# Kernel tuning notes

Hardware: AMD Instinct MI355X
Metric: run time of the kernel (lower is better)

## Reference

```python
import jax, jax.numpy as jnp
import numpy as np

BS = 128
E4M3_MAX = 448.0
E5M2_MAX = 57344.0


def qdq(x, fmax, dt):
    # block-wise (128-wide, last dim) fp8 quantize + dequantize (simulates act_quant + dequant in fp8_gemm)
    *lead, K = x.shape
    xb = x.reshape(*lead, K // BS, BS)
    s = jnp.maximum(jnp.max(jnp.abs(xb), axis=-1, keepdims=True) / fmax, 1e-12)
    xq = (xb / s).astype(dt).astype(jnp.float32)
    return (xq * s).reshape(*lead, K)


def fp8_linear(x, w, w_scale, fmax, dt, bias=None):
    # weight is fp8-valued (stored as f32 of the rounded values) with per-output-row-block scales
    x_dq = qdq(x, fmax, dt)
    sv = jnp.repeat(w_scale, BS)[: w.shape[0]]
    y = jnp.einsum('btk,ok->bto', x_dq, w * sv[:, None])
    return y if bias is None else y + bias


def fp8_ln(x, g, gs, b, bsc, eps=1e-5):
    mean = jnp.mean(x, axis=-1, keepdims=True)
    var = jnp.mean(jnp.square(x - mean), axis=-1, keepdims=True)  # unbiased=False
    xn = (x - mean) / jnp.sqrt(var + eps)
    d = x.shape[-1]
    return xn * (g * jnp.repeat(gs, BS)[:d]) + (b * jnp.repeat(bsc, BS)[:d])


def _fwd(x, attn_mask, wq, qs, wk, ks, wv, vs, wo, os_, fc1_w, fc1_s, fc1_b, fc2_w, fc2_s, fc2_b,
         ln1_g, ln1_gs, ln1_b, ln1_bs, ln2_g, ln2_gs, ln2_b, ln2_bs):
    B, T, C = x.shape
    H = 16
    HD = C // H
    e5 = jnp.float8_e5m2
    # attention (q/k/v/out projections use E5M2 fp8)
    q = fp8_linear(x, wq, qs, E5M2_MAX, e5).reshape(B, T, H, HD).transpose(0, 2, 1, 3)
    k = fp8_linear(x, wk, ks, E5M2_MAX, e5).reshape(B, T, H, HD).transpose(0, 2, 1, 3)
    v = fp8_linear(x, wv, vs, E5M2_MAX, e5).reshape(B, T, H, HD).transpose(0, 2, 1, 3)
    scores = jnp.einsum('bhqd,bhkd->bhqk', q, k) / jnp.sqrt(jnp.float32(HD))
    scores = jnp.where(attn_mask[:, None] == 0, -jnp.inf, scores)
    attn = jax.nn.softmax(scores, axis=-1)  # dropout = identity (eval)
    ctx = jnp.einsum('bhqk,bhkd->bhqd', attn, v).transpose(0, 2, 1, 3).reshape(B, T, C)
    attn_out = fp8_linear(ctx, wo, os_, E5M2_MAX, e5)
    x = fp8_ln(x + attn_out, ln1_g, ln1_gs, ln1_b, ln1_bs)
    # MLP (E4M3 fp8)
    e4 = jnp.float8_e4m3fn
    h = fp8_linear(x, fc1_w, fc1_s, E4M3_MAX, e4, fc1_b)
    h = jax.nn.gelu(h, approximate=False)  # torch nn.GELU default = exact erf
    ffn = fp8_linear(h, fc2_w, fc2_s, E4M3_MAX, e4, fc2_b)
    x = fp8_ln(x + ffn, ln2_g, ln2_gs, ln2_b, ln2_bs)
    return x


def _xavier_fp8(key, out_f, in_f, dt):
    bound = float(np.sqrt(6.0 / (in_f + out_f)))
    w = jax.random.uniform(key, (out_f, in_f), jnp.float32, -bound, bound)
    return w.astype(dt).astype(jnp.float32)  # simulate fp8 storage


def setup_inputs() -> dict:
    key = jax.random.key(0)
    kk = jax.random.split(key, 8)
    B, T, C, MLP = 2, 1024, 2048, 8192
    e5, e4 = jnp.float8_e5m2, jnp.float8_e4m3fn
    x = jax.random.normal(kk[0], (B, T, C), jnp.float32)
    attn_mask = jnp.broadcast_to(jnp.tril(jnp.ones((T, T), jnp.int32))[None], (B, T, T))
    nb = C // BS  # 16
    inp = {
        'x': x,
        'attn_mask': attn_mask,
        'wq': _xavier_fp8(kk[1], C, C, e5), 'qs': jnp.ones(nb, jnp.float32),
        'wk': _xavier_fp8(kk[2], C, C, e5), 'ks': jnp.ones(nb, jnp.float32),
        'wv': _xavier_fp8(kk[3], C, C, e5), 'vs': jnp.ones(nb, jnp.float32),
        'wo': _xavier_fp8(kk[4], C, C, e5), 'os_': jnp.ones(nb, jnp.float32),
        'fc1_w': _xavier_fp8(kk[5], MLP, C, e4), 'fc1_s': jnp.ones(MLP // BS, jnp.float32), 'fc1_b': jnp.zeros(MLP, jnp.float32),
        'fc2_w': _xavier_fp8(kk[6], C, MLP, e4), 'fc2_s': jnp.ones(nb, jnp.float32), 'fc2_b': jnp.zeros(C, jnp.float32),
        'ln1_g': jnp.ones(C, jnp.float32), 'ln1_gs': jnp.ones(nb, jnp.float32),
        'ln1_b': jnp.zeros(C, jnp.float32), 'ln1_bs': jnp.ones(nb, jnp.float32),
        'ln2_g': jnp.ones(C, jnp.float32), 'ln2_gs': jnp.ones(nb, jnp.float32),
        'ln2_b': jnp.zeros(C, jnp.float32), 'ln2_bs': jnp.ones(nb, jnp.float32),
    }
    return inp


def reference(x, attn_mask, wq, qs, wk, ks, wv, vs, wo, os_, fc1_w, fc1_s, fc1_b, fc2_w, fc2_s, fc2_b,
              ln1_g, ln1_gs, ln1_b, ln1_bs, ln2_g, ln2_gs, ln2_b, ln2_bs):
    return _fwd(x, attn_mask, wq, qs, wk, ks, wv, vs, wo, os_, fc1_w, fc1_s, fc1_b, fc2_w, fc2_s, fc2_b,
                ln1_g, ln1_gs, ln1_b, ln1_bs, ln2_g, ln2_gs, ln2_b, ln2_bs)
```

## Files before the change

### kernel.cpp

```cpp
#include <hip/hip_runtime.h>
#include <cstdint>


typedef __bf16 bf16x8 __attribute__((ext_vector_type(8)));
typedef unsigned short u16x8 __attribute__((ext_vector_type(8)));
typedef float f32x4 __attribute__((ext_vector_type(4)));
typedef float f32x16 __attribute__((ext_vector_type(16)));
typedef int i32x8 __attribute__((ext_vector_type(8)));
typedef unsigned short u16;

#if __has_builtin(__builtin_amdgcn_exp2f)
#define EXP2F(x) __builtin_amdgcn_exp2f(x)
#else
#define EXP2F(x) exp2f(x)
#endif

#define CFENCE() asm volatile("" ::: "memory")

__device__ __forceinline__ void gl_lds16(const void* g, void* l) {
  __builtin_amdgcn_global_load_lds(
      (const __attribute__((address_space(1))) void*)g,
      (__attribute__((address_space(3))) void*)l, 16, 0, 0);
}

struct u4x2 { uint4 a, b; };
__device__ __forceinline__ i32x8 pack8(uint4 lo, uint4 hi) {
  u4x2 t{lo, hi};
  return __builtin_bit_cast(i32x8, t);
}

__device__ __forceinline__ u16 bf16_rne(float v) {
  uint32_t u = __float_as_uint(v);
  u += 0x7FFFu + ((u >> 16) & 1u);
  return (u16)(u >> 16);
}

__device__ __forceinline__ float fp8_round(float v, int mbits, float minnorm, float subq) {
  float av = fabsf(v);
  if (av < minnorm) {
    return rintf(v / subq) * subq;
  }
  uint32_t u = __float_as_uint(v);
  const int shift = 23 - mbits;
  const uint32_t mask = (1u << shift) - 1u;
  const uint32_t rem = u & mask;
  uint32_t base = u & ~mask;
  const uint32_t half = 1u << (shift - 1);
  if (rem > half || (rem == half && ((base >> shift) & 1u))) base += (1u << shift);
  return __uint_as_float(base);
}

__device__ __forceinline__ uint8_t fp8_encode(float v, int mbits, int bias) {
  uint32_t u = __float_as_uint(v);
  uint32_t sign = (u >> 31) << 7;
  if ((u & 0x7FFFFFFFu) == 0) return (uint8_t)sign;
  int e = (int)((u >> 23) & 255u) - 127;
  if (e >= 1 - bias) {
    uint32_t mant = (u >> (23 - mbits)) & ((1u << mbits) - 1u);
    return (uint8_t)(sign | ((uint32_t)(e + bias) << mbits) | mant);
  }
  float q = fabsf(v) * __uint_as_float((uint32_t)(127 + bias - 1 + mbits) << 23);
  return (uint8_t)(sign | (uint32_t)q);
}

__global__ __launch_bounds__(256) void qdq_kernel(
    const float* __restrict__ x, uint8_t* __restrict__ q, float* __restrict__ sT,
    int nblk, int kbshift, float fmax, float minnorm, float subq, int mbits, int bias) {
  const int wid = blockIdx.x * 4 + (threadIdx.x >> 6);
  if (wid >= nblk) return;
  const int lane = threadIdx.x & 63;
  const size_t base = (size_t)wid * 128 + (size_t)lane * 2;
  float2 v = *(const float2*)(x + base);
  float am = fmaxf(fabsf(v.x), fabsf(v.y));
#pragma unroll
  for (int m = 32; m >= 1; m >>= 1) am = fmaxf(am, __shfl_xor(am, m));
  const float sc = fmaxf(am / fmax, 1e-12f);
  const float q0 = fp8_round(v.x / sc, mbits, minnorm, subq);
  const float q1 = fp8_round(v.y / sc, mbits, minnorm, subq);
  uchar2 o;
  o.x = fp8_encode(q0, mbits, bias);
  o.y = fp8_encode(q1, mbits, bias);
  *(uchar2*)(q + base) = o;
  if (lane == 0) {
    const int kbs = 1 << kbshift;
    const int m = wid >> kbshift;
    const int kb = wid & (kbs - 1);
    sT[(size_t)kb * (nblk >> kbshift) + m] = sc;
  }
}

__global__ __launch_bounds__(256) void w_to_fp8_kernel(
    const float* __restrict__ in, uint8_t* __restrict__ out, int n4, int mbits, int bias) {
  const int i = blockIdx.x * 256 + threadIdx.x;
  if (i >= n4) return;
  float4 v = ((const float4*)in)[i];
  uchar4 o;
  o.x = fp8_encode(v.x, mbits, bias);
  o.y = fp8_encode(v.y, mbits, bias);
  o.z = fp8_encode(v.z, mbits, bias);
  o.w = fp8_encode(v.w, mbits, bias);
  *(uchar4*)(out + (size_t)i * 4) = o;
}

__global__ void concat3_kernel(const float* __restrict__ a, const float* __restrict__ b,
                               const float* __restrict__ c, float* __restrict__ o, int n) {
  const int i = threadIdx.x;
  if (i < n) { o[i] = a[i]; o[n + i] = b[i]; o[2 * n + i] = c[i]; }
}

__global__ __launch_bounds__(256) void split_bf16_kernel(
    const float* __restrict__ in, u16* __restrict__ hi, u16* __restrict__ lo, int n4) {
  const int i = blockIdx.x * 256 + threadIdx.x;
  if (i >= n4) return;
  float4 v = ((const float4*)in)[i];
  float f[4] = {v.x, v.y, v.z, v.w};
  ushort4 oh, ol;
  u16* ph = (u16*)&oh;
  u16* pl = (u16*)&ol;
#pragma unroll
  for (int j = 0; j < 4; ++j) {
    u16 h = bf16_rne(f[j]);
    float hf = __uint_as_float((uint32_t)h << 16);
    ph[j] = h;
    pl[j] = bf16_rne(f[j] - hf);
  }
  ((ushort4*)hi)[i] = oh;
  ((ushort4*)lo)[i] = ol;
}

__global__ __launch_bounds__(256) void vtrans_kernel(
    const float* __restrict__ v, u16* __restrict__ vth, u16* __restrict__ vtl) {
  __shared__ float tile[64][65];
  const int tid = threadIdx.x;
  const int t0 = blockIdx.x * 64;
  const int d0 = blockIdx.y * 64;
  const int bh = blockIdx.z;
  const int b = bh >> 4, h = bh & 15;
#pragma unroll
  for (int s = 0; s < 4; ++s) {
    const int e = s * 256 + tid;
    const int r = e >> 4, c4 = e & 15;
    float4 val = *(const float4*)(v + ((size_t)(b * 1024 + t0 + r)) * 2048 + h * 128 + d0 + c4 * 4);
    tile[r][c4 * 4 + 0] = val.x;
    tile[r][c4 * 4 + 1] = val.y;
    tile[r][c4 * 4 + 2] = val.z;
    tile[r][c4 * 4 + 3] = val.w;
  }
  __syncthreads();
#pragma unroll
  for (int s = 0; s < 4; ++s) {
    const int e = s * 256 + tid;
    const int dr = e >> 4, tc4 = e & 15;
    ushort4 oh, ol;
    u16* ph = (u16*)&oh;
    u16* pl = (u16*)&ol;
#pragma unroll
    for (int i = 0; i < 4; ++i) {
      float f = tile[tc4 * 4 + i][dr];
      u16 hv = bf16_rne(f);
      ph[i] = hv;
      pl[i] = bf16_rne(f - __uint_as_float((uint32_t)hv << 16));
    }
    const size_t ob = ((size_t)(bh * 128 + d0 + dr)) * 1024 + t0 + tc4 * 4;
    *(ushort4*)(vth + ob) = oh;
    *(ushort4*)(vtl + ob) = ol;
  }
}

__global__ __launch_bounds__(256, 2) void attn_wave_kernel(
    const float* __restrict__ Q, const u16* __restrict__ Kh, const u16* __restrict__ Kl,
    const u16* __restrict__ Vth, const u16* __restrict__ Vtl, float* __restrict__ Octx) {
  constexpr int PLD = 34;
  __shared__ uint32_t Psm[4][32 * PLD];
  __shared__ float Osum[32 * 128];
  __shared__ float lsh[4][32];

  const int tid = threadIdx.x;
  const int w = tid >> 6;
  const int lane = tid & 63;
  const int l31 = lane & 31;
  const int q2 = lane >> 5;
  const int bh = blockIdx.x;
  const int b = bh >> 4;
  const int hofs = (bh & 15) * 128;
  const int qt = 31 - (int)blockIdx.y;
  const int i0 = qt * 32;
  const float SC2 = 0.12752698f;

  bf16x8 qh[8], ql[8];
  {
    const float* qp = Q + ((size_t)(b * 1024 + i0 + l31)) * 2048 + hofs + q2 * 8;
#pragma unroll
    for (int c = 0; c < 8; ++c) {
      float4 v0 = *(const float4*)(qp + c * 16);
      float4 v1 = *(const float4*)(qp + c * 16 + 4);
      float f[8] = {v0.x, v0.y, v0.z, v0.w, v1.x, v1.y, v1.z, v1.w};
      u16x8 uh, ul;
#pragma unroll
      for (int j = 0; j < 8; ++j) {
        u16 hv = bf16_rne(f[j]);
        uh[j] = hv;
        ul[j] = bf16_rne(f[j] - __uint_as_float((uint32_t)hv << 16));
      }
      qh[c] = __builtin_bit_cast(bf16x8, uh);
      ql[c] = __builtin_bit_cast(bf16x8, ul);
    }
  }

  const f32x16 z16 = {0.f};
  f32x16 Oacc[4] = {z16, z16, z16, z16};
  float lr[16];
#pragma unroll
  for (int r = 0; r < 16; ++r) lr[r] = 0.f;
  int rowq[16];
#pragma unroll
  for (int r = 0; r < 16; ++r) rowq[r] = (r & 3) + 8 * (r >> 2) + 4 * q2;

  uint32_t* Pw = Psm[w];
  for (int kt = w; kt <= qt; kt += 4) {
    const int j0 = kt * 32;
    const size_t krow = ((size_t)(b * 1024 + j0 + l31)) * 2048 + hofs + q2 * 8;
    f32x16 S = z16;
#pragma unroll
    for (int c = 0; c < 8; ++c) {
      bf16x8 k8h = *(const bf16x8*)(Kh + krow + c * 16);
      bf16x8 k8l = *(const bf16x8*)(Kl + krow + c * 16);
      S = __builtin_amdgcn_mfma_f32_32x32x16_bf16(qh[c], k8h, S, 0, 0, 0);
      S = __builtin_amdgcn_mfma_f32_32x32x16_bf16(qh[c], k8l, S, 0, 0, 0);
      S = __builtin_amdgcn_mfma_f32_32x32x16_bf16(ql[c], k8h, S, 0, 0, 0);
    }
    if (kt == qt) {
#pragma unroll
      for (int r = 0; r < 16; ++r)
        if (l31 > rowq[r]) S[r] = -3e38f;
    }
#pragma unroll
    for (int r = 0; r < 16; ++r) {
      const float p = EXP2F(S[r] * SC2);
      lr[r] += p;
      const u16 ph = bf16_rne(p);
      const u16 pl = bf16_rne(p - __uint_as_float((uint32_t)ph << 16));
      Pw[rowq[r] * PLD + l31] = (uint32_t)ph | ((uint32_t)pl << 16);
    }
#pragma unroll
    for (int s = 0; s < 2; ++s) {
      const uint32_t* rp = Pw + l31 * PLD + s * 16 + q2 * 8;
      uint2 a0 = *(const uint2*)(rp + 0);
      uint2 a1 = *(const uint2*)(rp + 2);
      uint2 a2 = *(const uint2*)(rp + 4);
      uint2 a3 = *(const uint2*)(rp + 6);
      u16x8 uh, ul;
      uh[0] = (u16)a0.x; ul[0] = (u16)(a0.x >> 16);
      uh[1] = (u16)a0.y; ul[1] = (u16)(a0.y >> 16);
      uh[2] = (u16)a1.x; ul[2] = (u16)(a1.x >> 16);
      uh[3] = (u16)a1.y; ul[3] = (u16)(a1.y >> 16);
      uh[4] = (u16)a2.x; ul[4] = (u16)(a2.x >> 16);
      uh[5] = (u16)a2.y; ul[5] = (u16)(a2.y >> 16);
      uh[6] = (u16)a3.x; ul[6] = (u16)(a3.x >> 16);
      uh[7] = (u16)a3.y; ul[7] = (u16)(a3.y >> 16);
      bf16x8 p8h = __builtin_bit_cast(bf16x8, uh);
      bf16x8 p8l = __builtin_bit_cast(bf16x8, ul);
      const size_t vrow = ((size_t)(bh * 128 + l31)) * 1024 + j0 + s * 16 + q2 * 8;
#pragma unroll
      for (int dt = 0; dt < 4; ++dt) {
        bf16x8 v8h = *(const bf16x8*)(Vth + vrow + (size_t)dt * 32768);
        bf16x8 v8l = *(const bf16x8*)(Vtl + vrow + (size_t)dt * 32768);
        Oacc[dt] = __builtin_amdgcn_mfma_f32_32x32x16_bf16(p8h, v8h, Oacc[dt], 0, 0, 0);
        Oacc[dt] = __builtin_amdgcn_mfma_f32_32x32x16_bf16(p8h, v8l, Oacc[dt], 0, 0, 0);
        Oacc[dt] = __builtin_amdgcn_mfma_f32_32x32x16_bf16(p8l, v8h, Oacc[dt], 0, 0, 0);
      }
    }
  }

#pragma unroll
  for (int r = 0; r < 16; ++r) {
    float t = lr[r];
    t += __shfl_xor(t, 1);
    t += __shfl_xor(t, 2);
    t += __shfl_xor(t, 4);
    t += __shfl_xor(t, 8);
    t += __shfl_xor(t, 16);
    lr[r] = t;
  }
  if (l31 == 0) {
#pragma unroll
    for (int r = 0; r < 16; ++r) lsh[w][rowq[r]] = lr[r];
  }
  if (w == 0) {
#pragma unroll
    for (int dt = 0; dt < 4; ++dt)
#pragma unroll
      for (int r = 0; r < 16; ++r) Osum[rowq[r] * 128 + dt * 32 + l31] = Oacc[dt][r];
  }
  __syncthreads();
  if (w == 1) {
#pragma unroll
    for (int dt = 0; dt < 4; ++dt)
#pragma unroll
      for (int r = 0; r < 16; ++r) Osum[rowq[r] * 128 + dt * 32 + l31] += Oacc[dt][r];
  }
  __syncthreads();
  if (w == 2) {
#pragma unroll
    for (int dt = 0; dt < 4; ++dt)
#pragma unroll
      for (int r = 0; r < 16; ++r) Osum[rowq[r] * 128 + dt * 32 + l31] += Oacc[dt][r];
  }
  __syncthreads();
  if (w == 3) {
#pragma unroll
    for (int dt = 0; dt < 4; ++dt)
#pragma unroll
      for (int r = 0; r < 16; ++r) Osum[rowq[r] * 128 + dt * 32 + l31] += Oacc[dt][r];
  }
  __syncthreads();
  const int row = w * 8 + (lane >> 3);
  const int c0 = (lane & 7) * 16;
  const float inv = 1.0f / (lsh[0][row] + lsh[1][row] + lsh[2][row] + lsh[3][row]);
  float* op = Octx + ((size_t)(b * 1024 + i0 + row)) * 2048 + hofs + c0;
#pragma unroll
  for (int i2 = 0; i2 < 4; ++i2) {
    float4 v = *(const float4*)(Osum + row * 128 + c0 + i2 * 4);
    v.x *= inv; v.y *= inv; v.z *= inv; v.w *= inv;
    *(float4*)(op + i2 * 4) = v;
  }
}

template <int FMT, int NK>
__global__ __launch_bounds__(256, (NK <= 16 ? 2 : 1)) void gemm_fp8_kernel(
    const uint8_t* __restrict__ A, const float* __restrict__ sxT,
    const uint8_t* __restrict__ W, const float* __restrict__ wsc,
    const float* __restrict__ bias, float* __restrict__ out,
    int M, int N, int K, int gelu, int seg_shift, int Nw) {
  __shared__ uint8_t As[2][16384];
  __shared__ uint8_t Ws[2][16384];
  __shared__ float sxs[NK * 128];

  const int tid = threadIdx.x;
  const int lane = tid & 63;
  const int wave = tid >> 6;
  const int wm = (wave >> 1) * 64;
  const int wn = (wave & 1) * 64;
  const int l31 = lane & 31;
  const int q2 = lane >> 5;
  const int bm = blockIdx.y * 128;
  const int bn = blockIdx.x * 128;

#pragma unroll
  for (int t = 0; t < NK * 128 / 1024; ++t) {
    const int e = t * 1024 + tid * 4;
    const int kt = e >> 7, r = e & 127;
    *(float4*)(sxs + e) = *(const float4*)(sxT + (size_t)kt * M + bm + r);
  }
  asm volatile("s_waitcnt vmcnt(0) lgkmcnt(0)" ::: "memory");
  __builtin_amdgcn_s_barrier();
  CFENCE();

  const int srow = wave * 8 + (lane >> 3);
  const int gchunk = (lane & 7) ^ (lane >> 3);
  const uint8_t* ga = A + (size_t)(bm + srow) * K + gchunk * 16;
  const uint8_t* gw = W + (size_t)(bn + srow) * K + gchunk * 16;
  const int lofs = srow * 128 + (lane & 7) * 16;

  const f32x16 z16 = {0.f};
  f32x16 acc[2][2] = {{z16, z16}, {z16, z16}};

#pragma unroll
  for (int s = 0; s < 4; ++s) {
    gl_lds16(ga + (size_t)s * 32 * K, &As[0][lofs + s * 4096]);
    gl_lds16(gw + (size_t)s * 32 * K, &Ws[0][lofs + s * 4096]);
  }
  ga += 128;
  gw += 128;
#pragma unroll
  for (int s = 0; s < 4; ++s) {
    gl_lds16(ga + (size_t)s * 32 * K, &As[1][lofs + s * 4096]);
    gl_lds16(gw + (size_t)s * 32 * K, &Ws[1][lofs + s * 4096]);
  }
  ga += 128;
  gw += 128;
  asm volatile("s_waitcnt vmcnt(8)" ::: "memory");
  __builtin_amdgcn_s_barrier();
  CFENCE();

  for (int kt = 0; kt < NK; ++kt) {
    const uint8_t* Asc = As[kt & 1];
    const uint8_t* Wsc = Ws[kt & 1];
    f32x16 chk[2][2] = {{z16, z16}, {z16, z16}};
#pragma unroll
    for (int mf = 0; mf < 2; ++mf) {
      i32x8 af[2], bf2[2];
      const int c = mf * 4 + q2 * 2;
#pragma unroll
      for (int i = 0; i < 2; ++i) {
        const int r = wm + i * 32 + l31;
        const uint8_t* Ar = Asc + r * 128;
        const int s7 = r & 7;
        af[i] = pack8(*(const uint4*)(Ar + ((c ^ s7) * 16)),
                      *(const uint4*)(Ar + (((c + 1) ^ s7) * 16)));
      }
#pragma unroll
      for (int j = 0; j < 2; ++j) {
        const int r = wn + j * 32 + l31;
        const uint8_t* Wr = Wsc + r * 128;
        const int s7 = r & 7;
        bf2[j] = pack8(*(const uint4*)(Wr + ((c ^ s7) * 16)),
                       *(const uint4*)(Wr + (((c + 1) ^ s7) * 16)));
      }
#pragma unroll
      for (int i = 0; i < 2; ++i)
#pragma unroll
        for (int j = 0; j < 2; ++j)
          chk[i][j] = __builtin_amdgcn_mfma_scale_f32_32x32x64_f8f6f4(
              af[i], bf2[j], chk[i][j], FMT, FMT, 0, 0x7F7F7F7F, 0, 0x7F7F7F7F);
    }
    const float* svl = sxs + kt * 128 + wm + q2 * 4;
#pragma unroll
    for (int i = 0; i < 2; ++i) {
#pragma unroll
      for (int rg = 0; rg < 4; ++rg) {
        const f32x4 sv = *(const f32x4*)(svl + i * 32 + rg * 8);
#pragma unroll
        for (int j = 0; j < 2; ++j)
#pragma unroll
          for (int rr = 0; rr < 4; ++rr)
            acc[i][j][rg * 4 + rr] += sv[rr] * chk[i][j][rg * 4 + rr];
      }
    }
    CFENCE();
    __builtin_amdgcn_s_barrier();
    CFENCE();
    if (kt + 1 < NK) {
      if (kt + 2 < NK) {
        uint8_t* Asn = As[kt & 1];
        uint8_t* Wsn = Ws[kt & 1];
#pragma unroll
        for (int s = 0; s < 4; ++s) {
          gl_lds16(ga + (size_t)s * 32 * K, Asn + lofs + s * 4096);
          gl_lds16(gw + (size_t)s * 32 * K, Wsn + lofs + s * 4096);
        }
        ga += 128;
        gw += 128;
        asm volatile("s_waitcnt vmcnt(8)" ::: "memory");
      } else {
        asm volatile("s_waitcnt vmcnt(0)" ::: "memory");
      }
      __builtin_amdgcn_s_barrier();
      CFENCE();
    }
  }

#pragma unroll
  for (int i = 0; i < 2; ++i) {
#pragma unroll
    for (int j = 0; j < 2; ++j) {
      const int n = bn + wn + j * 32 + l31;
      const float wsn = wsc[n >> 7];
      const float bv = bias ? bias[n] : 0.f;
      const int seg = n >> seg_shift;
      const int col = n & ((1 << seg_shift) - 1);
      float* op = out + (size_t)seg * M * Nw + col;
#pragma unroll
      for (int reg = 0; reg < 16; ++reg) {
        const int m = bm + wm + i * 32 + (reg & 3) + 8 * (reg >> 2) + 4 * q2;
        float v = acc[i][j][reg] * wsn + bv;
        if (gelu) v = 0.5f * v * (1.f + erff(v * 0.70710678118654752440f));
        op[(size_t)m * Nw] = v;
      }
    }
  }
}

__global__ __launch_bounds__(256) void ln_kernel(
    const float* __restrict__ a, const float* __restrict__ b2,
    const float* __restrict__ g, const float* __restrict__ gs,
    const float* __restrict__ bb, const float* __restrict__ bs,
    float* __restrict__ out, int C) {
  __shared__ float red[4];
  const int tid = threadIdx.x;
  const int row = blockIdx.x;
  const float* pa = a + (size_t)row * C;
  const float* pb = b2 + (size_t)row * C;
  float v[8];
  float sum = 0.f;
#pragma unroll
  for (int k = 0; k < 8; ++k) {
    const int c = tid + (k << 8);
    v[k] = pa[c] + pb[c];
    sum += v[k];
  }
#pragma unroll
  for (int m = 32; m >= 1; m >>= 1) sum += __shfl_xor(sum, m);
  if ((tid & 63) == 0) red[tid >> 6] = sum;
  __syncthreads();
  const float mean = (red[0] + red[1] + red[2] + red[3]) * (1.f / 2048.f);
  __syncthreads();
  float sq = 0.f;
#pragma unroll
  for (int k = 0; k < 8; ++k) {
    const float d = v[k] - mean;
    sq += d * d;
  }
#pragma unroll
  for (int m = 32; m >= 1; m >>= 1) sq += __shfl_xor(sq, m);
  if ((tid & 63) == 0) red[tid >> 6] = sq;
  __syncthreads();
  const float var = (red[0] + red[1] + red[2] + red[3]) * (1.f / 2048.f);
  const float inv = 1.0f / sqrtf(var + 1e-5f);
  float* po = out + (size_t)row * C;
#pragma unroll
  for (int k = 0; k < 8; ++k) {
    const int c = tid + (k << 8);
    po[c] = (v[k] - mean) * inv * (g[c] * gs[c >> 7]) + bb[c] * bs[c >> 7];
  }
}

extern "C" void kernel_launch(void* const* d_in, const int* in_sizes, int n_in,
                              void* d_out, int out_size, void* d_ws, size_t ws_size,
                              hipStream_t stream) {
  const int C = 2048, MLP = 8192;
  const int M = 2048;

  const float* x = (const float*)d_in[0];
  const float* wq = (const float*)d_in[2];
  const float* qs = (const float*)d_in[3];
  const float* wk = (const float*)d_in[4];
  const float* ks = (const float*)d_in[5];
  const float* wv = (const float*)d_in[6];
  const float* vs = (const float*)d_in[7];
  const float* wo = (const float*)d_in[8];
  const float* os_ = (const float*)d_in[9];
  const float* fc1_w = (const float*)d_in[10];
  const float* fc1_s = (const float*)d_in[11];
  const float* fc1_b = (const float*)d_in[12];
  const float* fc2_w = (const float*)d_in[13];
  const float* fc2_s = (const float*)d_in[14];
  const float* fc2_b = (const float*)d_in[15];
  const float* ln1_g = (const float*)d_in[16];
  const float* ln1_gs = (const float*)d_in[17];
  const float* ln1_b = (const float*)d_in[18];
  const float* ln1_bs = (const float*)d_in[19];
  const float* ln2_g = (const float*)d_in[20];
  const float* ln2_gs = (const float*)d_in[21];
  const float* ln2_b = (const float*)d_in[22];
  const float* ln2_bs = (const float*)d_in[23];

  char* ws = (char*)d_ws;
  const size_t o_Aq = 0;
  const size_t o_Wb = 33554432;
  const size_t o_sx = 67108864;
  const size_t o_ln1 = 67633152;
  const size_t o_q = 84410368;
  const size_t o_k = 101187584;
  const size_t o_v = 117964800;
  const size_t o_ctx = 134742016;
  const size_t o_attn = 151519232;
  const size_t o_h = o_q;
  const size_t o_ffn = o_attn;
  if (ws_size < 168296448ull) return;

  uint8_t* Aq = (uint8_t*)(ws + o_Aq);
  uint8_t* Wb = (uint8_t*)(ws + o_Wb);
  float* sx = (float*)(ws + o_sx);
  float* wsc3 = (float*)(ws + o_sx + 262144);
  float* ln1o = (float*)(ws + o_ln1);
  float* qb = (float*)(ws + o_q);
  float* kb = (float*)(ws + o_k);
  float* vb = (float*)(ws + o_v);
  float* ctx = (float*)(ws + o_ctx);
  float* attn_out = (float*)(ws + o_attn);
  float* hb = (float*)(ws + o_h);
  float* ffn = (float*)(ws + o_ffn);
  float* outp = (float*)d_out;
  u16* Kh = (u16*)(ws + o_Aq);
  u16* Kl = (u16*)(ws + o_Aq + 8388608);
  u16* Vth = (u16*)(ws + o_Aq + 16777216);
  u16* Vtl = (u16*)(ws + o_Aq + 25165824);

  const float E5_MAX = 57344.f, E5_MINN = 6.103515625e-05f, E5_SUBQ = 1.52587890625e-05f;
  const float E4_MAX = 448.f, E4_MINN = 0.015625f, E4_SUBQ = 0.001953125f;

  const dim3 blk(256);
  const int wc_qkv = (C * C / 4 + 255) / 256;
  const int wc_fc = (C * MLP / 4 + 255) / 256;

  qdq_kernel<<<M * (C / 128) / 4, blk, 0, stream>>>(x, Aq, sx, M * (C / 128), 4, E5_MAX, E5_MINN, E5_SUBQ, 2, 15);
  w_to_fp8_kernel<<<wc_qkv, blk, 0, stream>>>(wq, Wb, C * C / 4, 2, 15);
  w_to_fp8_kernel<<<wc_qkv, blk, 0, stream>>>(wk, Wb + C * C, C * C / 4, 2, 15);
  w_to_fp8_kernel<<<wc_qkv, blk, 0, stream>>>(wv, Wb + 2 * C * C, C * C / 4, 2, 15);
  concat3_kernel<<<1, 64, 0, stream>>>(qs, ks, vs, wsc3, C / 128);
  gemm_fp8_kernel<1, 16><<<dim3(3 * C / 128, M / 128), blk, 0, stream>>>(
      Aq, sx, Wb, wsc3, nullptr, qb, M, 3 * C, C, 0, 11, C);

  split_bf16_kernel<<<(M * C / 4 + 255) / 256, blk, 0, stream>>>(kb, Kh, Kl, M * C / 4);
  vtrans_kernel<<<dim3(16, 2, 32), blk, 0, stream>>>(vb, Vth, Vtl);
  attn_wave_kernel<<<dim3(32, 32), blk, 0, stream>>>(qb, Kh, Kl, Vth, Vtl, ctx);

  qdq_kernel<<<M * (C / 128) / 4, blk, 0, stream>>>(ctx, Aq, sx, M * (C / 128), 4, E5_MAX, E5_MINN, E5_SUBQ, 2, 15);
  w_to_fp8_kernel<<<wc_qkv, blk, 0, stream>>>(wo, Wb, C * C / 4, 2, 15);
  gemm_fp8_kernel<1, 16><<<dim3(C / 128, M / 128), blk, 0, stream>>>(
      Aq, sx, Wb, os_, nullptr, attn_out, M, C, C, 0, 30, C);

  ln_kernel<<<M, blk, 0, stream>>>(x, attn_out, ln1_g, ln1_gs, ln1_b, ln1_bs, ln1o, C);

  qdq_kernel<<<M * (C / 128) / 4, blk, 0, stream>>>(ln1o, Aq, sx, M * (C / 128), 4, E4_MAX, E4_MINN, E4_SUBQ, 3, 7);
  w_to_fp8_kernel<<<wc_fc, blk, 0, stream>>>(fc1_w, Wb, C * MLP / 4, 3, 7);
  gemm_fp8_kernel<0, 16><<<dim3(MLP / 128, M / 128), blk, 0, stream>>>(
      Aq, sx, Wb, fc1_s, fc1_b, hb, M, MLP, C, 1, 30, MLP);

  qdq_kernel<<<M * (MLP / 128) / 4, blk, 0, stream>>>(hb, Aq, sx, M * (MLP / 128), 6, E4_MAX, E4_MINN, E4_SUBQ, 3, 7);
  w_to_fp8_kernel<<<wc_fc, blk, 0, stream>>>(fc2_w, Wb, C * MLP / 4, 3, 7);
  gemm_fp8_kernel<0, 64><<<dim3(C / 128, M / 128), blk, 0, stream>>>(
      Aq, sx, Wb, fc2_s, fc2_b, ffn, M, C, MLP, 0, 30, C);

  ln_kernel<<<M, blk, 0, stream>>>(ln1o, ffn, ln2_g, ln2_gs, ln2_b, ln2_bs, outp, C);
}
```

Baseline: 701.7 us.

## Halve GEMM K-tile to 64 for higher occupancy; raise MFMA priority in attention

The fp8 GEMM now stages 64-byte K slices instead of 128, halving LDS per block. It uses a 2-bit XOR swizzle and forces two blocks per CU for every instantiation, including the fc2 NK=64 case. Each half-tile now takes its own barrier and scale-accumulate pass, so synchronisation and the fp32 rescale work double. In attention, s_setprio is raised around the MFMA groups so matrix instructions get issue priority over other waves.

```diff
diff --git a/kernel.cpp b/kernel.cpp
--- a/kernel.cpp
+++ b/kernel.cpp
@@ -225,9 +225,11 @@
     for (int c = 0; c < 8; ++c) {
       bf16x8 k8h = *(const bf16x8*)(Kh + krow + c * 16);
       bf16x8 k8l = *(const bf16x8*)(Kl + krow + c * 16);
+      __builtin_amdgcn_s_setprio(1);
       S = __builtin_amdgcn_mfma_f32_32x32x16_bf16(qh[c], k8h, S, 0, 0, 0);
       S = __builtin_amdgcn_mfma_f32_32x32x16_bf16(qh[c], k8l, S, 0, 0, 0);
       S = __builtin_amdgcn_mfma_f32_32x32x16_bf16(ql[c], k8h, S, 0, 0, 0);
+      __builtin_amdgcn_s_setprio(0);
     }
     if (kt == qt) {
 #pragma unroll
@@ -265,9 +267,11 @@
       for (int dt = 0; dt < 4; ++dt) {
         bf16x8 v8h = *(const bf16x8*)(Vth + vrow + (size_t)dt * 32768);
         bf16x8 v8l = *(const bf16x8*)(Vtl + vrow + (size_t)dt * 32768);
+        __builtin_amdgcn_s_setprio(1);
         Oacc[dt] = __builtin_amdgcn_mfma_f32_32x32x16_bf16(p8h, v8h, Oacc[dt], 0, 0, 0);
         Oacc[dt] = __builtin_amdgcn_mfma_f32_32x32x16_bf16(p8h, v8l, Oacc[dt], 0, 0, 0);
         Oacc[dt] = __builtin_amdgcn_mfma_f32_32x32x16_bf16(p8l, v8h, Oacc[dt], 0, 0, 0);
+        __builtin_amdgcn_s_setprio(0);
       }
     }
   }
@@ -327,13 +331,13 @@
 }
 
 template <int FMT, int NK>
-__global__ __launch_bounds__(256, (NK <= 16 ? 2 : 1)) void gemm_fp8_kernel(
+__global__ __launch_bounds__(256, 2) void gemm_db(
     const uint8_t* __restrict__ A, const float* __restrict__ sxT,
     const uint8_t* __restrict__ W, const float* __restrict__ wsc,
     const float* __restrict__ bias, float* __restrict__ out,
     int M, int N, int K, int gelu, int seg_shift, int Nw) {
-  __shared__ uint8_t As[2][16384];
-  __shared__ uint8_t Ws[2][16384];
+  __shared__ uint8_t As[2][128 * 64];
+  __shared__ uint8_t Ws[2][128 * 64];
   __shared__ float sxs[NK * 128];
 
   const int tid = threadIdx.x;
@@ -356,65 +360,63 @@
   __builtin_amdgcn_s_barrier();
   CFENCE();
 
-  const int srow = wave * 8 + (lane >> 3);
-  const int gchunk = (lane & 7) ^ (lane >> 3);
+  const int srow = wave * 32 + (lane >> 2);
+  const int gchunk = (lane & 3) ^ ((lane >> 2) & 3);
   const uint8_t* ga = A + (size_t)(bm + srow) * K + gchunk * 16;
   const uint8_t* gw = W + (size_t)(bn + srow) * K + gchunk * 16;
-  const int lofs = srow * 128 + (lane & 7) * 16;
+  const int lofs = wave * 2048 + lane * 16;
 
   const f32x16 z16 = {0.f};
   f32x16 acc[2][2] = {{z16, z16}, {z16, z16}};
 
 #pragma unroll
-  for (int s = 0; s < 4; ++s) {
-    gl_lds16(ga + (size_t)s * 32 * K, &As[0][lofs + s * 4096]);
-    gl_lds16(gw + (size_t)s * 32 * K, &Ws[0][lofs + s * 4096]);
-  }
-  ga += 128;
-  gw += 128;
-#pragma unroll
-  for (int s = 0; s < 4; ++s) {
-    gl_lds16(ga + (size_t)s * 32 * K, &As[1][lofs + s * 4096]);
-    gl_lds16(gw + (size_t)s * 32 * K, &Ws[1][lofs + s * 4096]);
-  }
-  ga += 128;
-  gw += 128;
-  asm volatile("s_waitcnt vmcnt(8)" ::: "memory");
+  for (int s = 0; s < 2; ++s) {
+    gl_lds16(ga + (size_t)s * 16 * K, &As[0][lofs + s * 1024]);
+    gl_lds16(gw + (size_t)s * 16 * K, &Ws[0][lofs + s * 1024]);
+  }
+  ga += 64;
+  gw += 64;
+#pragma unroll
+  for (int s = 0; s < 2; ++s) {
+    gl_lds16(ga + (size_t)s * 16 * K, &As[1][lofs + s * 1024]);
+    gl_lds16(gw + (size_t)s * 16 * K, &Ws[1][lofs + s * 1024]);
+  }
+  ga += 64;
+  gw += 64;
+  asm volatile("s_waitcnt vmcnt(4)" ::: "memory");
   __builtin_amdgcn_s_barrier();
   CFENCE();
 
-  for (int kt = 0; kt < NK; ++kt) {
-    const uint8_t* Asc = As[kt & 1];
-    const uint8_t* Wsc = Ws[kt & 1];
-    f32x16 chk[2][2] = {{z16, z16}, {z16, z16}};
-#pragma unroll
-    for (int mf = 0; mf < 2; ++mf) {
-      i32x8 af[2], bf2[2];
-      const int c = mf * 4 + q2 * 2;
-#pragma unroll
-      for (int i = 0; i < 2; ++i) {
-        const int r = wm + i * 32 + l31;
-        const uint8_t* Ar = Asc + r * 128;
-        const int s7 = r & 7;
-        af[i] = pack8(*(const uint4*)(Ar + ((c ^ s7) * 16)),
-                      *(const uint4*)(Ar + (((c + 1) ^ s7) * 16)));
-      }
-#pragma unroll
-      for (int j = 0; j < 2; ++j) {
-        const int r = wn + j * 32 + l31;
-        const uint8_t* Wr = Wsc + r * 128;
-        const int s7 = r & 7;
-        bf2[j] = pack8(*(const uint4*)(Wr + ((c ^ s7) * 16)),
-                       *(const uint4*)(Wr + (((c + 1) ^ s7) * 16)));
-      }
-#pragma unroll
-      for (int i = 0; i < 2; ++i)
-#pragma unroll
-        for (int j = 0; j < 2; ++j)
-          chk[i][j] = __builtin_amdgcn_mfma_scale_f32_32x32x64_f8f6f4(
-              af[i], bf2[j], chk[i][j], FMT, FMT, 0, 0x7F7F7F7F, 0, 0x7F7F7F7F);
-    }
-    const float* svl = sxs + kt * 128 + wm + q2 * 4;
+  const int NK2 = NK * 2;
+  for (int t = 0; t < NK2; ++t) {
+    const uint8_t* Asc = As[t & 1];
+    const uint8_t* Wsc = Ws[t & 1];
+    i32x8 af[2], bf2[2];
+    const int c0 = q2 * 2;
+#pragma unroll
+    for (int i = 0; i < 2; ++i) {
+      const int r = wm + i * 32 + l31;
+      const uint8_t* Ar = Asc + r * 64;
+      const int s3 = r & 3;
+      af[i] = pack8(*(const uint4*)(Ar + ((c0 ^ s3) * 16)),
+                    *(const uint4*)(Ar + (((c0 + 1) ^ s3) * 16)));
+    }
+#pragma unroll
+    for (int j = 0; j < 2; ++j) {
+      const int r = wn + j * 32 + l31;
+      const uint8_t* Wr = Wsc + r * 64;
+      const int s3 = r & 3;
+      bf2[j] = pack8(*(const uint4*)(Wr + ((c0 ^ s3) * 16)),
+                     *(const uint4*)(Wr + (((c0 + 1) ^ s3) * 16)));
+    }
+    f32x16 chk[2][2];
+#pragma unroll
+    for (int i = 0; i < 2; ++i)
+#pragma unroll
+      for (int j = 0; j < 2; ++j)
+        chk[i][j] = __builtin_amdgcn_mfma_scale_f32_32x32x64_f8f6f4(
+            af[i], bf2[j], z16, FMT, FMT, 0, 0x7F7F7F7F, 0, 0x7F7F7F7F);
+    const float* svl = sxs + (t >> 1) * 128 + wm + q2 * 4;
 #pragma unroll
     for (int i = 0; i < 2; ++i) {
 #pragma unroll
@@ -430,18 +432,18 @@
     CFENCE();
     __builtin_amdgcn_s_barrier();
     CFENCE();
-    if (kt + 1 < NK) {
-      if (kt + 2 < NK) {
-        uint8_t* Asn = As[kt & 1];
-        uint8_t* Wsn = Ws[kt & 1];
-#pragma unroll
-        for (int s = 0; s < 4; ++s) {
-          gl_lds16(ga + (size_t)s * 32 * K, Asn + lofs + s * 4096);
-          gl_lds16(gw + (size_t)s * 32 * K, Wsn + lofs + s * 4096);
+    if (t + 1 < NK2) {
+      if (t + 2 < NK2) {
+        uint8_t* Asn = &As[t & 1][lofs];
+        uint8_t* Wsn = &Ws[t & 1][lofs];
+#pragma unroll
+        for (int s = 0; s < 2; ++s) {
+          gl_lds16(ga + (size_t)s * 16 * K, Asn + s * 1024);
+          gl_lds16(gw + (size_t)s * 16 * K, Wsn + s * 1024);
         }
-        ga += 128;
-        gw += 128;
-        asm volatile("s_waitcnt vmcnt(8)" ::: "memory");
+        ga += 64;
+        gw += 64;
+        asm volatile("s_waitcnt vmcnt(4)" ::: "memory");
       } else {
         asm volatile("s_waitcnt vmcnt(0)" ::: "memory");
       }
@@ -589,7 +591,7 @@
   w_to_fp8_kernel<<<wc_qkv, blk, 0, stream>>>(wk, Wb + C * C, C * C / 4, 2, 15);
   w_to_fp8_kernel<<<wc_qkv, blk, 0, stream>>>(wv, Wb + 2 * C * C, C * C / 4, 2, 15);
   concat3_kernel<<<1, 64, 0, stream>>>(qs, ks, vs, wsc3, C / 128);
-  gemm_fp8_kernel<1, 16><<<dim3(3 * C / 128, M / 128), blk, 0, stream>>>(
+  gemm_db<1, 16><<<dim3(3 * C / 128, M / 128), blk, 0, stream>>>(
       Aq, sx, Wb, wsc3, nullptr, qb, M, 3 * C, C, 0, 11, C);
 
   split_bf16_kernel<<<(M * C / 4 + 255) / 256, blk, 0, stream>>>(kb, Kh, Kl, M * C / 4);
@@ -598,19 +600,19 @@
 
   qdq_kernel<<<M * (C / 128) / 4, blk, 0, stream>>>(ctx, Aq, sx, M * (C / 128), 4, E5_MAX, E5_MINN, E5_SUBQ, 2, 15);
   w_to_fp8_kernel<<<wc_qkv, blk, 0, stream>>>(wo, Wb, C * C / 4, 2, 15);
-  gemm_fp8_kernel<1, 16><<<dim3(C / 128, M / 128), blk, 0, stream>>>(
+  gemm_db<1, 16><<<dim3(C / 128, M / 128), blk, 0, stream>>>(
       Aq, sx, Wb, os_, nullptr, attn_out, M, C, C, 0, 30, C);
 
   ln_kernel<<<M, blk, 0, stream>>>(x, attn_out, ln1_g, ln1_gs, ln1_b, ln1_bs, ln1o, C);
 
   qdq_kernel<<<M * (C / 128) / 4, blk, 0, stream>>>(ln1o, Aq, sx, M * (C / 128), 4, E4_MAX, E4_MINN, E4_SUBQ, 3, 7);
   w_to_fp8_kernel<<<wc_fc, blk, 0, stream>>>(fc1_w, Wb, C * MLP / 4, 3, 7);
-  gemm_fp8_kernel<0, 16><<<dim3(MLP / 128, M / 128), blk, 0, stream>>>(
+  gemm_db<0, 16><<<dim3(MLP / 128, M / 128), blk, 0, stream>>>(
       Aq, sx, Wb, fc1_s, fc1_b, hb, M, MLP, C, 1, 30, MLP);
 
   qdq_kernel<<<M * (MLP / 128) / 4, blk, 0, stream>>>(hb, Aq, sx, M * (MLP / 128), 6, E4_MAX, E4_MINN, E4_SUBQ, 3, 7);
   w_to_fp8_kernel<<<wc_fc, blk, 0, stream>>>(fc2_w, Wb, C * MLP / 4, 3, 7);
-  gemm_fp8_kernel<0, 64><<<dim3(C / 128, M / 128), blk, 0, stream>>>(
+  gemm_db<0, 64><<<dim3(C / 128, M / 128), blk, 0, stream>>>(
       Aq, sx, Wb, fc2_s, fc2_b, ffn, M, C, MLP, 0, 30, C);
 
   ln_kernel<<<M, blk, 0, stream>>>(ln1o, ffn, ln2_g, ln2_gs, ln2_b, ln2_bs, outp, C);
```

After: 695.2 us. About the same (-0.9%).
